# Kernel optimization log

Hardware: AMD Instinct MI355X
Metric: run time of the kernel (lower is better)

The kernel has to match this reference:

```python
import jax, jax.numpy as jnp
import numpy as np


def setup_inputs() -> dict:
    key = jax.random.key(0)
    k1, k2, k3 = jax.random.split(key, 3)
    B, L, H = 8, 2048, 256
    g = jax.random.normal(k1, (B, L, H), dtype=jnp.float32)
    # nn.Linear weights: stored as [out_features, in_features]
    WP = jax.random.normal(k2, (H, H), dtype=jnp.float32) * (1.0 / np.sqrt(H))
    W_out = jax.random.normal(k3, (H, 3 * H), dtype=jnp.float32) * (1.0 / np.sqrt(3 * H))
    b_out = jnp.zeros((H,), dtype=jnp.float32)
    return {"g": g, "WP": WP, "W_out": W_out, "b_out": b_out}


def reference(g, WP, W_out, b_out):
    # Wh = WP(g): [B, L, H] @ WP^T
    Wh = jnp.einsum("blh,oh->blo", g, WP)
    # s_t = bmm(Wh, g^T): [B, L, L]  (rows indexed by Wh positions, cols by g positions)
    s_t = jnp.einsum("bih,bjh->bij", Wh, g)
    # softmax over dim=1 (the first L axis, non-standard)
    a_t = jax.nn.softmax(s_t, axis=1)
    # c_t = bmm(a_t, g): [B, L, H]
    c_t = jnp.einsum("bij,bjh->bih", a_t, g)
    out = jnp.concatenate((g, c_t, g * c_t), axis=2)  # [B, L, 3H]
    out = jnp.einsum("blk,ok->blo", out, W_out) + b_out
    return jax.nn.relu(out)
```

## Files before the change

### kernel.cpp

```cpp
#include <hip/hip_runtime.h>
#include <math.h>

static constexpr int  Bb = 8;
static constexpr int  L  = 2048;
static constexpr int  H  = 256;
static constexpr long BL = (long)Bb * L;
static constexpr long LH = (long)L * H;
static constexpr long LL = (long)L * L;
static constexpr int  NCH = 16;

typedef __attribute__((ext_vector_type(8))) unsigned short u16x8;
typedef __attribute__((ext_vector_type(4))) unsigned short u16x4;
typedef __attribute__((ext_vector_type(8))) _Float16       f16x8;
typedef __attribute__((ext_vector_type(4))) float          f32x4;

__device__ __forceinline__ unsigned short f2hu(float x) {
    union { _Float16 h; unsigned short u; } v; v.h = (_Float16)x; return v.u;
}
__device__ __forceinline__ float hu2f(unsigned short u) {
    union { unsigned short u; _Float16 h; } v; v.u = u; return (float)v.h;
}
__device__ __forceinline__ void gl_lds16(const unsigned short* g, unsigned short* l) {
    __builtin_amdgcn_global_load_lds(
        (const __attribute__((address_space(1))) unsigned int*)g,
        (__attribute__((address_space(3))) unsigned int*)l, 16, 0, 0);
}

__global__ __launch_bounds__(256)
void cvt_g(const float* __restrict__ x, unsigned short* __restrict__ h)
{
    const long i = ((long)blockIdx.x * 256 + threadIdx.x) * 4;
    float4 v = *(const float4*)(x + i);
    u16x4 o;
    o[0] = f2hu(v.x); o[1] = f2hu(v.y); o[2] = f2hu(v.z); o[3] = f2hu(v.w);
    *(u16x4*)(h + i) = o;
}

__global__ __launch_bounds__(256)
void cvt_two(const float* __restrict__ x1, unsigned short* __restrict__ h1,
             const float* __restrict__ x2, unsigned short* __restrict__ h2)
{
    const float* x; unsigned short* hp; long base;
    if (blockIdx.x < 64) { x = x1; hp = h1; base = (long)blockIdx.x * 1024; }
    else { x = x2; hp = h2; base = (long)(blockIdx.x - 64) * 1024; }
    const long i = base + (long)threadIdx.x * 4;
    float4 v = *(const float4*)(x + i);
    u16x4 o;
    o[0] = f2hu(v.x); o[1] = f2hu(v.y); o[2] = f2hu(v.z); o[3] = f2hu(v.w);
    *(u16x4*)(hp + i) = o;
}

__global__ __launch_bounds__(256)
void transpose_h16(const unsigned short* __restrict__ in, unsigned short* __restrict__ outf)
{
    __shared__ unsigned short T[32][33];
    const int b = blockIdx.z, j0 = blockIdx.x * 32, h0 = blockIdx.y * 32;
    const int t = threadIdx.x, r = t >> 3, c4 = (t & 7) << 2;
    const unsigned short* inb = in + (long)b * LH;
    unsigned short* ob = outf + (long)b * LH;
    u16x4 v = *(const u16x4*)(inb + (long)(j0 + r) * H + h0 + c4);
#pragma unroll
    for (int e = 0; e < 4; ++e) T[r][c4 + e] = v[e];
    __syncthreads();
    const int f = t >> 7, lam = (t & 127) >> 1, half = t & 1;
    const int hloc  = f * 16 + (lam & 15);
    const int jbase = half * 16 + (lam >> 4) * 4;
    u16x4 o;
#pragma unroll
    for (int d = 0; d < 4; ++d) o[d] = T[jbase + d][hloc];
    *(u16x4*)(ob + ((long)((h0 >> 4) + f) * (L / 32) + (j0 >> 5)) * 512
                 + lam * 8 + half * 4) = o;
}

__global__ __launch_bounds__(256)
void col_stats_r(const float* __restrict__ pm, const float* __restrict__ pz,
                 unsigned short* __restrict__ r16)
{
    const long idx = (long)blockIdx.x * 256 + threadIdx.x;
    const long b = idx / L, j = idx - b * L;
    const float* pmb = pm + b * (long)NCH * L + j;
    const float* pzb = pz + b * (long)NCH * L + j;
    float m = -1e30f;
#pragma unroll
    for (int c = 0; c < NCH; ++c) m = fmaxf(m, pmb[(long)c * L]);
    float z = 0.f;
#pragma unroll
    for (int c = 0; c < NCH; ++c) z += pzb[(long)c * L] * __expf(pmb[(long)c * L] - m);
    const float zi = 1.f / z;
    unsigned short* rb = r16 + b * (long)NCH * L + j;
#pragma unroll
    for (int c = 0; c < NCH; ++c) rb[(long)c * L] = f2hu(__expf(pmb[(long)c * L] - m) * zi);
}

template<int MODE, int NSEG>
__global__ __launch_bounds__(256)
void mfma_nt(const unsigned short* A0, const unsigned short* A1, const unsigned short* A2,
             const unsigned short* B0, const unsigned short* B1, const unsigned short* B2,
             float* __restrict__ C, unsigned short* __restrict__ Ch,
             float* __restrict__ pm, float* __restrict__ pz,
             const float* __restrict__ bias,
             int N, int lda, int ldb,
             long strideA, long strideB, long strideC)
{
    __shared__ __align__(16) unsigned short As[128][32];
    __shared__ __align__(16) unsigned short Bs[128][32];
    __shared__ float smx[2][128];
    __shared__ float szx[2][128];
    __shared__ float colm[128];
    const int tid  = threadIdx.x;
    const int wid  = tid >> 6, lane = tid & 63;
    const int wm   = wid >> 1, wn = wid & 1;
    const long b   = blockIdx.z;
    const int m0   = blockIdx.x * 128, n0 = blockIdx.y * 128;
    const int lrow = tid >> 2, lkc = (tid & 3) << 3;
    const int frow = lane & 15, fk = (lane >> 4) << 3;
    f32x4 acc[4][4];
#pragma unroll
    for (int i = 0; i < 4; ++i)
#pragma unroll
        for (int j = 0; j < 4; ++j) acc[i][j] = (f32x4){0.f, 0.f, 0.f, 0.f};

    const long abase = b * strideA, bbase = b * strideB;
    unsigned short* AsW = &As[0][0] + ((tid >> 6) << 9);
    unsigned short* BsW = &Bs[0][0] + ((tid >> 6) << 9);

    for (int seg = 0; seg < NSEG; ++seg) {
        const unsigned short* Ap = (seg == 0) ? A0 : ((seg == 1) ? A1 : A2);
        const unsigned short* Bp = (seg == 0) ? B0 : ((seg == 1) ? B1 : B2);
        for (int k0 = 0; k0 < 256; k0 += 32) {
            if (MODE == 1) {
                __syncthreads();
#pragma unroll
                for (int r = 0; r < 2; ++r) {
                    const int row = lrow + (r << 6);
                    u16x8 av;
                    if (seg == 2) {
                        const long off = (long)(m0 + row) * lda + k0 + lkc;
                        u16x8 gv = *(const u16x8*)(A0 + off);
                        u16x8 cv = *(const u16x8*)(A1 + off);
#pragma unroll
                        for (int e = 0; e < 8; ++e)
                            av[e] = f2hu(hu2f(gv[e]) * hu2f(cv[e]));
                    } else {
                        av = *(const u16x8*)(Ap + (long)(m0 + row) * lda + k0 + lkc);
                    }
                    *(u16x8*)&As[row][lkc] = av;
                    u16x8 bv = *(const u16x8*)(Bp + (long)(n0 + row) * ldb + k0 + lkc);
                    *(u16x8*)&Bs[row][lkc] = bv;
                }
                __syncthreads();
            } else {
                const unsigned short* Abase = Ap + abase + (long)m0 * lda + k0;
                const unsigned short* Bbase = Bp + bbase + (long)n0 * ldb + k0;
                __syncthreads();
#pragma unroll
                for (int r = 0; r < 2; ++r) {
                    gl_lds16(Abase + (long)(lrow + (r << 6)) * lda + lkc, AsW + (r << 11));
                    gl_lds16(Bbase + (long)(lrow + (r << 6)) * ldb + lkc, BsW + (r << 11));
                }
                __syncthreads();
            }
            f16x8 af[4], bfv[4];
#pragma unroll
            for (int i = 0; i < 4; ++i) af[i]  = *(const f16x8*)&As[wm * 64 + i * 16 + frow][fk];
#pragma unroll
            for (int j = 0; j < 4; ++j) bfv[j] = *(const f16x8*)&Bs[wn * 64 + j * 16 + frow][fk];
#pragma unroll
            for (int i = 0; i < 4; ++i)
#pragma unroll
                for (int j = 0; j < 4; ++j)
                    acc[i][j] = __builtin_amdgcn_mfma_f32_16x16x32_f16(af[i], bfv[j], acc[i][j], 0, 0, 0);
        }
    }

    if (MODE == 0) {
        const int q = lane >> 4, c16 = lane & 15;
        float rm[4][4];
#pragma unroll
        for (int ja = 0; ja < 4; ++ja)
#pragma unroll
            for (int e = 0; e < 4; ++e) {
                float m = fmaxf(fmaxf(acc[ja][0][e], acc[ja][1][e]),
                                fmaxf(acc[ja][2][e], acc[ja][3][e]));
                m = fmaxf(m, __shfl_xor(m, 1));
                m = fmaxf(m, __shfl_xor(m, 2));
                m = fmaxf(m, __shfl_xor(m, 4));
                m = fmaxf(m, __shfl_xor(m, 8));
                rm[ja][e] = m;
            }
        if (c16 == 0) {
#pragma unroll
            for (int ja = 0; ja < 4; ++ja)
#pragma unroll
                for (int e = 0; e < 4; ++e)
                    smx[wn][wm * 64 + ja * 16 + q * 4 + e] = rm[ja][e];
        }
        __syncthreads();
        if (tid < 128) colm[tid] = fmaxf(smx[0][tid], smx[1][tid]);
        __syncthreads();
        unsigned short* Pt = Ch + b * strideC;
#pragma unroll
        for (int ja = 0; ja < 4; ++ja) {
            float mm[4];
#pragma unroll
            for (int e = 0; e < 4; ++e) mm[e] = colm[wm * 64 + ja * 16 + q * 4 + e];
            float zr[4] = {0.f, 0.f, 0.f, 0.f};
#pragma unroll
            for (int ib = 0; ib < 4; ++ib) {
                u16x4 pv;
#pragma unroll
                for (int e = 0; e < 4; ++e) {
                    float p = __expf(acc[ja][ib][e] - mm[e]);
                    zr[e] += p;
                    pv[e] = f2hu(p);
                }
                const long ti = (n0 >> 4) + wn * 4 + ib;
                const long tj = (m0 >> 4) + wm * 4 + ja;
                *(u16x4*)(Pt + (ti * (L / 16) + tj) * 256 + lane * 4) = pv;
            }
#pragma unroll
            for (int e = 0; e < 4; ++e) {
                float z = zr[e];
                z += __shfl_xor(z, 1); z += __shfl_xor(z, 2);
                z += __shfl_xor(z, 4); z += __shfl_xor(z, 8);
                if (c16 == 0) szx[wn][wm * 64 + ja * 16 + q * 4 + e] = z;
            }
        }
        __syncthreads();
        if (tid < 128) {
            const long o = ((long)b * NCH + blockIdx.y) * L + m0 + tid;
            pm[o] = colm[tid];
            pz[o] = szx[0][tid] + szx[1][tid];
        }
    } else {
#pragma unroll
        for (int i = 0; i < 4; ++i)
#pragma unroll
            for (int j = 0; j < 4; ++j) {
                const int rbase = m0 + wm * 64 + i * 16 + ((lane >> 4) << 2);
                const int col   = n0 + wn * 64 + j * 16 + frow;
                if (MODE == 2) {
#pragma unroll
                    for (int e = 0; e < 4; ++e)
                        Ch[(long)(rbase + e) * N + col] = f2hu(acc[i][j][e]);
                } else {
                    float* Cb = C + b * strideC;
                    const float bv = bias[col];
#pragma unroll
                    for (int e = 0; e < 4; ++e)
                        Cb[(long)(rbase + e) * N + col] = fmaxf(acc[i][j][e] + bv, 0.f);
                }
            }
    }
}

__global__ __launch_bounds__(256)
void attn_av(const unsigned short* __restrict__ P, const unsigned short* __restrict__ r16,
             const unsigned short* __restrict__ gTf, unsigned short* __restrict__ ch)
{
    const int t = threadIdx.x, b = blockIdx.z;
    const int i0 = blockIdx.x * 32;
    const int w = t >> 6, l = t & 63, q = l >> 4, c16 = l & 15;
    const unsigned short* Pb0 = P + (long)b * LL + ((long)(i0 >> 4) * 128) * 256 + l * 4;
    const unsigned short* Pb1 = Pb0 + 128 * 256;
    const unsigned short* rb  = r16 + ((long)b * NCH + (i0 >> 7)) * L;
    const unsigned short* Bb0 = gTf + (long)b * LH + ((long)(w * 4) * 64) * 512 + l * 8;
    unsigned short* cb = ch + (long)b * LH;

    f32x4 acc[2][4];
#pragma unroll
    for (int i = 0; i < 2; ++i)
#pragma unroll
        for (int j = 0; j < 4; ++j) acc[i][j] = (f32x4){0.f, 0.f, 0.f, 0.f};

#pragma unroll 2
    for (int s = 0; s < 64; ++s) {
        union { u16x4 u[2]; f16x8 h; } a0v, a1v, rv;
        a0v.u[0] = *(const u16x4*)(Pb0 + (2 * s    ) * 256);
        a0v.u[1] = *(const u16x4*)(Pb0 + (2 * s + 1) * 256);
        a1v.u[0] = *(const u16x4*)(Pb1 + (2 * s    ) * 256);
        a1v.u[1] = *(const u16x4*)(Pb1 + (2 * s + 1) * 256);
        rv.u[0]  = *(const u16x4*)(rb + s * 32 + q * 4);
        rv.u[1]  = *(const u16x4*)(rb + s * 32 + 16 + q * 4);
        f16x8 a0 = a0v.h * rv.h;
        f16x8 a1 = a1v.h * rv.h;
#pragma unroll
        for (int j4 = 0; j4 < 4; ++j4) {
            u16x8 bu = *(const u16x8*)(Bb0 + ((long)j4 * 64 + s) * 512);
            f16x8 bf = *(f16x8*)&bu;
            acc[0][j4] = __builtin_amdgcn_mfma_f32_16x16x32_f16(a0, bf, acc[0][j4], 0, 0, 0);
            acc[1][j4] = __builtin_amdgcn_mfma_f32_16x16x32_f16(a1, bf, acc[1][j4], 0, 0, 0);
        }
    }

#pragma unroll
    for (int i = 0; i < 2; ++i)
#pragma unroll
        for (int j = 0; j < 4; ++j) {
            const int rbase = i0 + i * 16 + q * 4;
            const int col   = w * 64 + j * 16 + c16;
#pragma unroll
            for (int e = 0; e < 4; ++e)
                cb[(long)(rbase + e) * H + col] = f2hu(acc[i][j][e]);
        }
}

extern "C" void kernel_launch(void* const* d_in, const int* in_sizes, int n_in,
                              void* d_out, int out_size, void* d_ws, size_t ws_size,
                              hipStream_t stream)
{
    const float* g     = (const float*)d_in[0];
    const float* WP    = (const float*)d_in[1];
    const float* W_out = (const float*)d_in[2];
    const float* b_out = (const float*)d_in[3];
    float* out = (float*)d_out;

    char* w = (char*)d_ws;
    unsigned short* P    = (unsigned short*)w;
    unsigned short* gh   = (unsigned short*)(w + 67108864);
    unsigned short* ch   = (unsigned short*)(w + 75497472);
    unsigned short* gTf  = (unsigned short*)(w + 83886080);
    unsigned short* Whh  = (unsigned short*)(w + 92274688);
    unsigned short* WPh  = (unsigned short*)(w + 100663296);
    unsigned short* Woh  = (unsigned short*)(w + 100794368);
    float*          pm   = (float*)(w + 101187584);
    float*          pz   = (float*)(w + 102236160);
    unsigned short* r16  = (unsigned short*)(w + 103284736);

    cvt_g<<<dim3((int)(BL * H / 1024)), 256, 0, stream>>>(g, gh);
    cvt_two<<<dim3(256), 256, 0, stream>>>(WP, WPh, W_out, Woh);

    mfma_nt<2, 1><<<dim3((int)(BL / 128), H / 128, 1), 256, 0, stream>>>(
        gh, nullptr, nullptr, WPh, nullptr, nullptr, nullptr, Whh,
        nullptr, nullptr, nullptr, H, H, H, 0, 0, 0);

    mfma_nt<0, 1><<<dim3(L / 128, L / 128, Bb), 256, 0, stream>>>(
        gh, nullptr, nullptr, Whh, nullptr, nullptr, nullptr, P,
        pm, pz, nullptr, L, H, H, LH, LH, LL);

    col_stats_r<<<dim3((int)(BL / 256)), 256, 0, stream>>>(pm, pz, r16);

    transpose_h16<<<dim3(L / 32, H / 32, Bb), 256, 0, stream>>>(gh, gTf);

    attn_av<<<dim3(L / 32, 1, Bb), 256, 0, stream>>>(P, r16, gTf, ch);

    mfma_nt<1, 3><<<dim3((int)(BL / 128), H / 128, 1), 256, 0, stream>>>(
        gh, ch, nullptr, Woh, Woh + 256, Woh + 512, out, nullptr,
        nullptr, nullptr, b_out, H, H, 3 * H, 0, 0, 0);
}
```

Before: 201.6 us.

## Fuse g conversion with transpose and double-buffer LDS loads in MFMA GEMM

```diff
diff --git a/kernel.cpp b/kernel.cpp
--- a/kernel.cpp
+++ b/kernel.cpp
@@ -27,13 +27,29 @@
 }
 
 __global__ __launch_bounds__(256)
-void cvt_g(const float* __restrict__ x, unsigned short* __restrict__ h)
-{
-    const long i = ((long)blockIdx.x * 256 + threadIdx.x) * 4;
-    float4 v = *(const float4*)(x + i);
+void cvt_g_t(const float* __restrict__ g, unsigned short* __restrict__ gh,
+             unsigned short* __restrict__ gTf)
+{
+    __shared__ unsigned short T[32][33];
+    const int b = blockIdx.z, j0 = blockIdx.x * 32, h0 = blockIdx.y * 32;
+    const int t = threadIdx.x, r = t >> 3, c4 = (t & 7) << 2;
+    const long off = (long)b * LH + (long)(j0 + r) * H + h0 + c4;
+    float4 v = *(const float4*)(g + off);
     u16x4 o;
     o[0] = f2hu(v.x); o[1] = f2hu(v.y); o[2] = f2hu(v.z); o[3] = f2hu(v.w);
-    *(u16x4*)(h + i) = o;
+    *(u16x4*)(gh + off) = o;
+#pragma unroll
+    for (int e = 0; e < 4; ++e) T[r][c4 + e] = o[e];
+    __syncthreads();
+    unsigned short* ob = gTf + (long)b * LH;
+    const int f = t >> 7, lam = (t & 127) >> 1, half = t & 1;
+    const int hloc  = f * 16 + (lam & 15);
+    const int jbase = half * 16 + (lam >> 4) * 4;
+    u16x4 w;
+#pragma unroll
+    for (int d = 0; d < 4; ++d) w[d] = T[jbase + d][hloc];
+    *(u16x4*)(ob + ((long)((h0 >> 4) + f) * (L / 32) + (j0 >> 5)) * 512
+                 + lam * 8 + half * 4) = w;
 }
 
 __global__ __launch_bounds__(256)
@@ -51,28 +67,6 @@
 }
 
 __global__ __launch_bounds__(256)
-void transpose_h16(const unsigned short* __restrict__ in, unsigned short* __restrict__ outf)
-{
-    __shared__ unsigned short T[32][33];
-    const int b = blockIdx.z, j0 = blockIdx.x * 32, h0 = blockIdx.y * 32;
-    const int t = threadIdx.x, r = t >> 3, c4 = (t & 7) << 2;
-    const unsigned short* inb = in + (long)b * LH;
-    unsigned short* ob = outf + (long)b * LH;
-    u16x4 v = *(const u16x4*)(inb + (long)(j0 + r) * H + h0 + c4);
-#pragma unroll
-    for (int e = 0; e < 4; ++e) T[r][c4 + e] = v[e];
-    __syncthreads();
-    const int f = t >> 7, lam = (t & 127) >> 1, half = t & 1;
-    const int hloc  = f * 16 + (lam & 15);
-    const int jbase = half * 16 + (lam >> 4) * 4;
-    u16x4 o;
-#pragma unroll
-    for (int d = 0; d < 4; ++d) o[d] = T[jbase + d][hloc];
-    *(u16x4*)(ob + ((long)((h0 >> 4) + f) * (L / 32) + (j0 >> 5)) * 512
-                 + lam * 8 + half * 4) = o;
-}
-
-__global__ __launch_bounds__(256)
 void col_stats_r(const float* __restrict__ pm, const float* __restrict__ pz,
                  unsigned short* __restrict__ r16)
 {
@@ -102,8 +96,9 @@
              int N, int lda, int ldb,
              long strideA, long strideB, long strideC)
 {
-    __shared__ __align__(16) unsigned short As[128][32];
-    __shared__ __align__(16) unsigned short Bs[128][32];
+    constexpr int DB = (MODE == 1) ? 1 : 2;
+    __shared__ __align__(16) unsigned short As[DB][128][32];
+    __shared__ __align__(16) unsigned short Bs[DB][128][32];
     __shared__ float smx[2][128];
     __shared__ float szx[2][128];
     __shared__ float colm[128];
@@ -121,14 +116,12 @@
         for (int j = 0; j < 4; ++j) acc[i][j] = (f32x4){0.f, 0.f, 0.f, 0.f};
 
     const long abase = b * strideA, bbase = b * strideB;
-    unsigned short* AsW = &As[0][0] + ((tid >> 6) << 9);
-    unsigned short* BsW = &Bs[0][0] + ((tid >> 6) << 9);
-
-    for (int seg = 0; seg < NSEG; ++seg) {
-        const unsigned short* Ap = (seg == 0) ? A0 : ((seg == 1) ? A1 : A2);
-        const unsigned short* Bp = (seg == 0) ? B0 : ((seg == 1) ? B1 : B2);
-        for (int k0 = 0; k0 < 256; k0 += 32) {
-            if (MODE == 1) {
+
+    if (MODE == 1) {
+        for (int seg = 0; seg < NSEG; ++seg) {
+            const unsigned short* Ap = (seg == 0) ? A0 : ((seg == 1) ? A1 : A2);
+            const unsigned short* Bp = (seg == 0) ? B0 : ((seg == 1) ? B1 : B2);
+            for (int k0 = 0; k0 < 256; k0 += 32) {
                 __syncthreads();
 #pragma unroll
                 for (int r = 0; r < 2; ++r) {
@@ -144,33 +137,64 @@
                     } else {
                         av = *(const u16x8*)(Ap + (long)(m0 + row) * lda + k0 + lkc);
                     }
-                    *(u16x8*)&As[row][lkc] = av;
+                    *(u16x8*)&As[0][row][lkc] = av;
                     u16x8 bv = *(const u16x8*)(Bp + (long)(n0 + row) * ldb + k0 + lkc);
-                    *(u16x8*)&Bs[row][lkc] = bv;
+                    *(u16x8*)&Bs[0][row][lkc] = bv;
                 }
                 __syncthreads();
-            } else {
-                const unsigned short* Abase = Ap + abase + (long)m0 * lda + k0;
-                const unsigned short* Bbase = Bp + bbase + (long)n0 * ldb + k0;
-                __syncthreads();
-#pragma unroll
-                for (int r = 0; r < 2; ++r) {
-                    gl_lds16(Abase + (long)(lrow + (r << 6)) * lda + lkc, AsW + (r << 11));
-                    gl_lds16(Bbase + (long)(lrow + (r << 6)) * ldb + lkc, BsW + (r << 11));
-                }
-                __syncthreads();
-            }
+                f16x8 af[4], bfv[4];
+#pragma unroll
+                for (int i = 0; i < 4; ++i) af[i]  = *(const f16x8*)&As[0][wm * 64 + i * 16 + frow][fk];
+#pragma unroll
+                for (int j = 0; j < 4; ++j) bfv[j] = *(const f16x8*)&Bs[0][wn * 64 + j * 16 + frow][fk];
+#pragma unroll
+                for (int i = 0; i < 4; ++i)
+#pragma unroll
+                    for (int j = 0; j < 4; ++j)
+                        acc[i][j] = __builtin_amdgcn_mfma_f32_16x16x32_f16(af[i], bfv[j], acc[i][j], 0, 0, 0);
+            }
+        }
+    } else {
+        const unsigned short* Abase = A0 + abase + (long)m0 * lda;
+        const unsigned short* Bbase = B0 + bbase + (long)n0 * ldb;
+        unsigned short* AsW = &As[0][0][0] + ((tid >> 6) << 9);
+        unsigned short* BsW = &Bs[0][0][0] + ((tid >> 6) << 9);
+
+#define STG(BUF, KO)                                                         \
+        {                                                                    \
+            _Pragma("unroll")                                                \
+            for (int r = 0; r < 2; ++r) {                                    \
+                gl_lds16(Abase + (long)(lrow + (r << 6)) * lda + (KO) + lkc, \
+                         AsW + (BUF) * 4096 + (r << 11));                    \
+                gl_lds16(Bbase + (long)(lrow + (r << 6)) * ldb + (KO) + lkc, \
+                         BsW + (BUF) * 4096 + (r << 11));                    \
+            }                                                                \
+        }
+
+        STG(0, 0)
+        asm volatile("s_waitcnt vmcnt(0)" ::: "memory");
+        __builtin_amdgcn_s_barrier();
+        __builtin_amdgcn_sched_barrier(0);
+
+#pragma unroll
+        for (int ks = 0; ks < 8; ++ks) {
+            const int cur = ks & 1;
+            if (ks < 7) STG(cur ^ 1, (ks + 1) * 32)
             f16x8 af[4], bfv[4];
 #pragma unroll
-            for (int i = 0; i < 4; ++i) af[i]  = *(const f16x8*)&As[wm * 64 + i * 16 + frow][fk];
-#pragma unroll
-            for (int j = 0; j < 4; ++j) bfv[j] = *(const f16x8*)&Bs[wn * 64 + j * 16 + frow][fk];
+            for (int i = 0; i < 4; ++i) af[i]  = *(const f16x8*)&As[cur][wm * 64 + i * 16 + frow][fk];
+#pragma unroll
+            for (int j = 0; j < 4; ++j) bfv[j] = *(const f16x8*)&Bs[cur][wn * 64 + j * 16 + frow][fk];
 #pragma unroll
             for (int i = 0; i < 4; ++i)
 #pragma unroll
                 for (int j = 0; j < 4; ++j)
                     acc[i][j] = __builtin_amdgcn_mfma_f32_16x16x32_f16(af[i], bfv[j], acc[i][j], 0, 0, 0);
-        }
+            if (ks < 7) { asm volatile("s_waitcnt vmcnt(0)" ::: "memory"); }
+            __builtin_amdgcn_s_barrier();
+            __builtin_amdgcn_sched_barrier(0);
+        }
+#undef STG
     }
 
     if (MODE == 0) {
@@ -327,7 +351,7 @@
     float*          pz   = (float*)(w + 102236160);
     unsigned short* r16  = (unsigned short*)(w + 103284736);
 
-    cvt_g<<<dim3((int)(BL * H / 1024)), 256, 0, stream>>>(g, gh);
+    cvt_g_t<<<dim3(L / 32, H / 32, Bb), 256, 0, stream>>>(g, gh, gTf);
     cvt_two<<<dim3(256), 256, 0, stream>>>(WP, WPh, W_out, Woh);
 
     mfma_nt<2, 1><<<dim3((int)(BL / 128), H / 128, 1), 256, 0, stream>>>(
@@ -340,8 +364,6 @@
 
     col_stats_r<<<dim3((int)(BL / 256)), 256, 0, stream>>>(pm, pz, r16);
 
-    transpose_h16<<<dim3(L / 32, H / 32, Bb), 256, 0, stream>>>(gh, gTf);
-
     attn_av<<<dim3(L / 32, 1, Bb), 256, 0, stream>>>(P, r16, gTf, ch);
 
     mfma_nt<1, 3><<<dim3((int)(BL / 128), H / 128, 1), 256, 0, stream>>>(
```

New measurement: 201.3 us. Within noise of the previous version (-0.2%).
